# Performance work log

Hardware: AMD Instinct MI355X
Metric: run time of the kernel (lower is better)

The kernel has to match this reference:

```python
import jax, jax.numpy as jnp
import numpy as np
from jax import lax

PART = 224   # PART_IMAGE_SIZE
PAD = 224    # PAD_SIZE
TOPN = 4
IOU_THRESH = 0.25
N_ANCHORS = 1614


def _conv(x, w, b, stride, pad):
    y = lax.conv_general_dilated(x, w, (stride, stride), [(pad, pad), (pad, pad)],
                                 dimension_numbers=('NCHW', 'OIHW', 'NCHW'))
    return y + b[None, :, None, None]


def _iou(box, boxes):
    # box [4], boxes [N,4] as (y0,x0,y1,x1)
    yy0 = jnp.maximum(box[0], boxes[:, 0]); xx0 = jnp.maximum(box[1], boxes[:, 1])
    yy1 = jnp.minimum(box[2], boxes[:, 2]); xx1 = jnp.minimum(box[3], boxes[:, 3])
    inter = jnp.clip(yy1 - yy0, 0.0) * jnp.clip(xx1 - xx0, 0.0)
    a = (box[2] - box[0]) * (box[3] - box[1])
    areas = (boxes[:, 2] - boxes[:, 0]) * (boxes[:, 3] - boxes[:, 1])
    return inter / (a + areas - inter)


def _nms(scores, boxes):
    # hard NMS keeping TOPN boxes; returns indices [TOPN]
    valid = jnp.ones(scores.shape, dtype=bool)
    idxs = []
    for _ in range(TOPN):
        i = jnp.argmax(jnp.where(valid, scores, -jnp.inf))
        idxs.append(i)
        valid = valid & (_iou(boxes[i], boxes) <= IOU_THRESH)
    return jnp.stack(idxs)


def _crop_resize(img, box):
    # img [3,Hp,Wp] padded image, box [4] float; bilinear, align_corners=True,
    # matching F.interpolate(x_pad[:, :, y0:y1, x0:x1], (PART, PART))
    Hp, Wp = img.shape[1], img.shape[2]
    def coords(c0, c1, L):
        t = jnp.arange(PART, dtype=img.dtype) / (PART - 1)
        c = c0 + (c1 - 1.0 - c0) * t          # absolute source coordinate
        cf = jnp.floor(c)
        lo = jnp.clip(cf.astype(jnp.int32), 0, L - 1)
        hi = jnp.clip(lo + 1, 0, L - 1)
        return lo, hi, c - cf
    yl, yh, wy = coords(box[0], box[2], Hp)
    xl, xh, wx = coords(box[1], box[3], Wp)
    g = lambda yi, xi: img[:, yi[:, None], xi[None, :]]   # [3,PART,PART]
    return ((1 - wy)[:, None] * ((1 - wx) * g(yl, xl) + wx * g(yl, xh))
            + wy[:, None] * ((1 - wx) * g(yh, xl) + wx * g(yh, xh)))


def setup_inputs() -> dict:
    key = jax.random.key(0)
    ks = jax.random.split(key, 20)
    x = jax.random.uniform(ks[0], (16, 3, 448, 448), dtype=jnp.float32)
    rpn_feature = jax.random.normal(ks[1], (16, 2048, 14, 14), dtype=jnp.float32)
    # valid boxes inside the padded 896x896 image
    y0 = jax.random.randint(ks[2], (N_ANCHORS,), 0, 560)
    x0 = jax.random.randint(ks[3], (N_ANCHORS,), 0, 560)
    h = jax.random.randint(ks[4], (N_ANCHORS,), 32, 336)
    w = jax.random.randint(ks[5], (N_ANCHORS,), 32, 336)
    anchors = jnp.stack([y0, x0, jnp.minimum(y0 + h, 896), jnp.minimum(x0 + w, 896)], axis=1).astype(jnp.int32)
    s = 0.02
    inp = {
        'x': x, 'rpn_feature': rpn_feature, 'anchors': anchors,
        'w_down1': jax.random.normal(ks[6], (128, 2048, 3, 3), jnp.float32) * s,
        'b_down1': jnp.zeros((128,), jnp.float32),
        'w_down2': jax.random.normal(ks[7], (128, 128, 3, 3), jnp.float32) * s,
        'b_down2': jnp.zeros((128,), jnp.float32),
        'w_down3': jax.random.normal(ks[8], (128, 128, 3, 3), jnp.float32) * s,
        'b_down3': jnp.zeros((128,), jnp.float32),
        'w_tidy1': jax.random.normal(ks[9], (6, 128, 1, 1), jnp.float32) * s,
        'b_tidy1': jnp.zeros((6,), jnp.float32),
        'w_tidy2': jax.random.normal(ks[10], (6, 128, 1, 1), jnp.float32) * s,
        'b_tidy2': jnp.zeros((6,), jnp.float32),
        'w_tidy3': jax.random.normal(ks[11], (9, 128, 1, 1), jnp.float32) * s,
        'b_tidy3': jnp.zeros((9,), jnp.float32),
    }
    return inp


def reference(x, rpn_feature, anchors,
              w_down1, b_down1, w_down2, b_down2, w_down3, b_down3,
              w_tidy1, b_tidy1, w_tidy2, b_tidy2, w_tidy3, b_tidy3):
    B = x.shape[0]
    # ProposalNet
    d1 = jax.nn.relu(_conv(rpn_feature, w_down1, b_down1, 1, 1))   # [B,128,14,14]
    d2 = jax.nn.relu(_conv(d1, w_down2, b_down2, 2, 1))            # [B,128,7,7]
    d3 = jax.nn.relu(_conv(d2, w_down3, b_down3, 2, 1))            # [B,128,4,4]
    t1 = _conv(d1, w_tidy1, b_tidy1, 1, 0).reshape(B, -1)
    t2 = _conv(d2, w_tidy2, b_tidy2, 1, 0).reshape(B, -1)
    t3 = _conv(d3, w_tidy3, b_tidy3, 1, 0).reshape(B, -1)
    rpn_score = jnp.concatenate([t1, t2, t3], axis=1)              # [B, 1614]
    boxes = anchors.astype(x.dtype)                                # [N,4]
    top_n_index = jax.vmap(lambda s: _nms(s, boxes))(rpn_score)    # [B,TOPN]
    top_n_prob = jnp.take_along_axis(rpn_score, top_n_index, axis=1)
    x_pad = jnp.pad(x, ((0, 0), (0, 0), (PAD, PAD), (PAD, PAD)))   # [B,3,896,896]
    sel_boxes = boxes[top_n_index]                                 # [B,TOPN,4]
    part_imgs = jax.vmap(lambda img, bxs: jax.vmap(lambda b: _crop_resize(img, b))(bxs))(x_pad, sel_boxes)
    # part_imgs: [B,TOPN,3,PART,PART]
    return rpn_score, top_n_index, top_n_prob, part_imgs
```

## Files before the change

### kernel.cpp

```cpp
#include <hip/hip_runtime.h>
#include <hip/hip_bf16.h>

#define NB 16
#define NA 1614
#define NBP (NB * 196 * 128)
#define NBP2 (NB * 128 * 49)

typedef __bf16 bf16x8 __attribute__((ext_vector_type(8)));
typedef float f32x4 __attribute__((ext_vector_type(4)));

__device__ __forceinline__ unsigned short f2bf(float v) {
  unsigned u = __float_as_uint(v);
  unsigned r = (u + 0x7FFFu + ((u >> 16) & 1u)) >> 16;
  return (unsigned short)r;
}
__device__ __forceinline__ float bf2f(unsigned short s) {
  return __uint_as_float(((unsigned)s) << 16);
}

__global__ __launch_bounds__(256)
void prep(const float* __restrict__ w, const float* __restrict__ in,
          unsigned short* __restrict__ wTh, unsigned short* __restrict__ wTl,
          unsigned short* __restrict__ aTh, unsigned short* __restrict__ aTl) {
  __shared__ float sbuf[32 * 289];
  const int bid = blockIdx.x;
  if (bid < 1024) {
    const int chunk = bid & 63, b = bid >> 6;
    const float* src = in + ((size_t)b * 2048 + chunk * 32) * 196;
#pragma unroll
    for (int r = 0; r < 7; r++) {
      int e = threadIdx.x + 256 * r;
      if (e < 1568) {
        int ic = e / 49, f = e - ic * 49;
        float4 v = ((const float4*)(src + (size_t)ic * 196))[f];
        float* d = sbuf + ic * 201 + f * 4;
        d[0] = v.x; d[1] = v.y; d[2] = v.z; d[3] = v.w;
      }
    }
    __syncthreads();
    unsigned short* oh = aTh + (size_t)bid * (196 * 32);
    unsigned short* ol = aTl + (size_t)bid * (196 * 32);
#pragma unroll
    for (int r = 0; r < 4; r++) {
      int e = threadIdx.x + 256 * r;
      if (e < 784) {
        int pos = e >> 2, part = e & 3;
        unsigned short hv[8], lv[8];
#pragma unroll
        for (int j = 0; j < 8; j++) {
          float v = sbuf[(part * 8 + j) * 201 + pos];
          unsigned short h = f2bf(v);
          hv[j] = h;
          lv[j] = f2bf(v - bf2f(h));
        }
        ((uint4*)oh)[e] = *(uint4*)hv;
        ((uint4*)ol)[e] = *(uint4*)lv;
      }
    }
  } else {
    const int bid2 = bid - 1024;
    const int ocg = bid2 & 3, ks = (bid2 >> 2) & 3, kcp = bid2 >> 4;
    const int oc0 = ocg * 32;
    const int ic0 = kcp * 128 + ks * 32;
#pragma unroll
    for (int r = 0; r < 9; r++) {
      int f = threadIdx.x + 256 * r;
      int o = f / 72, rem4 = f - o * 72;
      float4 v = *(const float4*)(w + ((size_t)(oc0 + o) * 2048 + ic0) * 9 + rem4 * 4);
      float* d = sbuf + o * 289 + rem4 * 4;
      d[0] = v.x; d[1] = v.y; d[2] = v.z; d[3] = v.w;
    }
    __syncthreads();
#pragma unroll
    for (int r = 0; r < 36; r++) {
      int e = threadIdx.x + 256 * r;
      int tap = e >> 10, rem = e & 1023;
      int o = rem >> 5, ic = rem & 31;
      float v = sbuf[o * 289 + ic * 9 + tap];
      unsigned short h = f2bf(v);
      size_t g2 = ((size_t)(kcp * 36 + tap * 4 + ks) << 12) + oc0 * 32 + rem;
      wTh[g2] = h;
      wTl[g2] = f2bf(v - bf2f(h));
    }
  }
}

#define APL 1360
#define ABUF (4 * APL)

#define LOADB(H, L, T, K)                                                     \
  {                                                                           \
    const size_t o_ = ((size_t)(kc * 36 + (T) * 4 + (K)) << 12) + bln;        \
    const unsigned short* ph_ = wTh + o_;                                     \
    const unsigned short* pq_ = wTl + o_;                                     \
    H[0] = *(const bf16x8*)(ph_);                                             \
    H[1] = *(const bf16x8*)(ph_ + 512);                                       \
    L[0] = *(const bf16x8*)(pq_);                                             \
    L[1] = *(const bf16x8*)(pq_ + 512);                                       \
  }

#define STEP(IT, BUH, BUL, BNH, BNL)                                          \
  {                                                                           \
    const int it_ = (IT);                                                     \
    const int ks_ = it_ / 9, tap_ = it_ - ks_ * 9;                            \
    {             \
      const int ni_ = (it_ < 35) ? it_ + 1 : 35;                              \
      const int nk_ = ni_ / 9, nt_ = ni_ - nk_ * 9;                           \
      LOADB(BNH, BNL, nt_, nk_);                                              \
    }                                                                         \
    if (ks_ < 3) {        \
      if (tap_ == 3 || tap_ == 4) {                                           \
        int e_ = tid + 256 * (tap_ - 3);                                      \
        if (e_ < ne) {                                                        \
          int u_ = pos04 + e_;                                                \
          int pos_ = u_ >> 2, part_ = u_ & 3;                                 \
          int py_ = pos_ / 14, px_ = pos_ - py_ * 14;                         \
          int d_ = (((ks_ + 1) & 1) ? ABUF : 0) + part_ * APL                 \
                   + (py_ + 1 - rowoff) * 136 + (px_ + 1) * 8;                \
          *(uint4*)(sAh + d_) = sgh;                                          \
          *(uint4*)(sAl + d_) = sgl;                                          \
        }                                                                     \
      }                                                                       \
      if (tap_ == 2 || tap_ == 3) {                                           \
        const uint4* gh_ = (const uint4*)(aTh + ((size_t)(b * 64 + kc * 4 + ks_ + 1) * 196) * 32); \
        const uint4* gl_ = (const uint4*)(aTl + ((size_t)(b * 64 + kc * 4 + ks_ + 1) * 196) * 32); \
        int e_ = tid + 256 * (tap_ - 2);                                      \
        if (e_ < ne) { sgh = gh_[pos04 + e_]; sgl = gl_[pos04 + e_]; }        \
      }                                                                       \
    }                                                                         \
    const int t8_ = (tap_ / 3) * 136 + (tap_ - (tap_ / 3) * 3) * 8;           \
    const unsigned short* pah_ = sAh + (ks_ & 1) * ABUF + qoff + t8_;         \
    const unsigned short* pal_ = sAl + (ks_ & 1) * ABUF + qoff + t8_;         \
    bf16x8 afh[7], afl[7];                                                    \
    _Pragma("unroll") for (int mf = 0; mf < 7; mf++) {                        \
      afh[mf] = *(const bf16x8*)(pah_ + abase[mf]);                           \
      afl[mf] = *(const bf16x8*)(pal_ + abase[mf]);                           \
    }                                                                         \
    _Pragma("unroll") for (int mf = 0; mf < 7; mf++)                          \
      _Pragma("unroll") for (int nf = 0; nf < 2; nf++)                        \
        acc[mf][nf] = __builtin_amdgcn_mfma_f32_16x16x32_bf16(afh[mf], BUH[nf], acc[mf][nf], 0, 0, 0); \
    _Pragma("unroll") for (int mf = 0; mf < 7; mf++)                          \
      _Pragma("unroll") for (int nf = 0; nf < 2; nf++)                        \
        acc[mf][nf] = __builtin_amdgcn_mfma_f32_16x16x32_bf16(afl[mf], BUH[nf], acc[mf][nf], 0, 0, 0); \
    _Pragma("unroll") for (int mf = 0; mf < 7; mf++)                          \
      _Pragma("unroll") for (int nf = 0; nf < 2; nf++)                        \
        acc[mf][nf] = __builtin_amdgcn_mfma_f32_16x16x32_bf16(afh[mf], BUL[nf], acc[mf][nf], 0, 0, 0); \
    if (tap_ == 8) __syncthreads();                                           \
  }

__global__ __launch_bounds__(256, 2)
void conv1_mfma(const unsigned short* __restrict__ aTh, const unsigned short* __restrict__ aTl,
                const unsigned short* __restrict__ wTh, const unsigned short* __restrict__ wTl,
                float* __restrict__ p1) {
  const int bid = blockIdx.x;
  const int kc = bid & 15;
  const int b  = (bid >> 4) & 15;
  const int mh = bid >> 8;
  const int tid = threadIdx.x;
  const int wid = tid >> 6, lane = tid & 63;
  const int wn = wid;
  const int q = lane >> 4, ln = lane & 15;

  __shared__ unsigned short sAh[2 * ABUF];
  __shared__ unsigned short sAl[2 * ABUF];

  const int rowoff = 6 * mh;
  const int pos0 = mh ? 98 : 0;
  const int ne   = mh ? 392 : 504;
  const int pos04 = pos0 * 4;

  for (int e = tid; e < 2 * ABUF / 2; e += 256) {
    ((unsigned int*)sAh)[e] = 0u;
    ((unsigned int*)sAl)[e] = 0u;
  }

  int abase[7];
#pragma unroll
  for (int mf = 0; mf < 7; mf++) {
    int row = mh * 112 + mf * 16 + ln;
    int y = row / 14, x = row - y * 14;
    abase[mf] = (row < 196) ? ((y - rowoff) * 136 + x * 8) : 0;
  }
  const int qoff = q * APL;
  const int bln = (wn * 32 + ln) * 32 + q * 8;

  f32x4 acc[7][2];
#pragma unroll
  for (int mf = 0; mf < 7; mf++)
#pragma unroll
    for (int nf = 0; nf < 2; nf++) acc[mf][nf] = (f32x4){0.f, 0.f, 0.f, 0.f};

  uint4 sgh = {}, sgl = {};

  __syncthreads();

  {
    const uint4* gh = (const uint4*)(aTh + ((size_t)(b * 64 + kc * 4) * 196) * 32);
    const uint4* gl = (const uint4*)(aTl + ((size_t)(b * 64 + kc * 4) * 196) * 32);
#pragma unroll
    for (int r = 0; r < 2; r++) {
      int e = tid + 256 * r;
      if (e < ne) {
        int u = pos04 + e;
        int pos = u >> 2, part = u & 3;
        int py = pos / 14, px = pos - py * 14;
        int d = part * APL + (py + 1 - rowoff) * 136 + (px + 1) * 8;
        *(uint4*)(sAh + d) = gh[u];
        *(uint4*)(sAl + d) = gl[u];
      }
    }
  }
  bf16x8 b0h[2], b0l[2], b1h[2], b1l[2];
  LOADB(b0h, b0l, 0, 0);
  __syncthreads();

  for (int it = 0; it < 36; it += 2) {
    STEP(it,     b0h, b0l, b1h, b1l);
    STEP(it + 1, b1h, b1l, b0h, b0l);
  }

  float* pk = p1 + ((size_t)kc * NB + b) * 196 * 128;
#pragma unroll
  for (int mf = 0; mf < 7; mf++) {
    const int row0 = mh * 112 + mf * 16 + q * 4;
#pragma unroll
    for (int nf = 0; nf < 2; nf++) {
      const int oc = wn * 32 + nf * 16 + ln;
#pragma unroll
      for (int r = 0; r < 4; r++) {
        const int row = row0 + r;
        if (row < 196) pk[(size_t)row * 128 + oc] = acc[mf][nf][r];
      }
    }
  }
}

__global__ __launch_bounds__(256)
void conv1_finish_p(const float* __restrict__ p1, const float* __restrict__ bias,
                    float* __restrict__ d1) {
  __shared__ float s[7 * 132];
  const int bid = blockIdx.x;
  const int pt = bid % 28, b = bid / 28;
  const int tid = threadIdx.x;
  if (tid < 224) {
    int pos = tid >> 5, oc4 = tid & 31;
    const float* base = p1 + ((size_t)(b * 196 + pt * 7 + pos)) * 128 + oc4 * 4;
    float4 sum = ((const float4*)bias)[oc4];
#pragma unroll
    for (int k = 0; k < 16; k++) {
      float4 v = *(const float4*)(base + (size_t)k * NBP);
      sum.x += v.x; sum.y += v.y; sum.z += v.z; sum.w += v.w;
    }
    sum.x = fmaxf(sum.x, 0.f); sum.y = fmaxf(sum.y, 0.f);
    sum.z = fmaxf(sum.z, 0.f); sum.w = fmaxf(sum.w, 0.f);
    *(float4*)(s + pos * 132 + oc4 * 4) = sum;
  }
  __syncthreads();
#pragma unroll
  for (int r = 0; r < 4; r++) {
    int e = tid + 256 * r;
    if (e < 896) {
      int oc = e / 7, f = e - oc * 7;
      d1[((size_t)b * 128 + oc) * 196 + pt * 7 + f] = s[f * 132 + oc];
    }
  }
}

__global__ void conv2_part(const float* __restrict__ d1, const float* __restrict__ w,
                           float* __restrict__ p2) {
  const int bid = blockIdx.x;
  const int kc = bid & 3, oct = (bid >> 2) & 3, b = bid >> 4;
  const int ic0 = kc * 32, oc0 = oct * 32;
  const int tid = threadIdx.x;
  const int ocl = tid >> 3, rw = tid & 7;

  __shared__ float s_in[32 * 320];
  __shared__ float s_w[32 * 324];

#pragma unroll
  for (int r = 0; r < 32; r++) {
    const int e = tid + 256 * r;
    const int ch = e >> 8, idx = e & 255;
    const int tr = idx >> 4, tc = idx & 15;
    const int iy = tr - 1, ix = tc - 1;
    float v = 0.f;
    if ((unsigned)iy < 14u && (unsigned)ix < 14u)
      v = d1[((size_t)b * 128 + ic0 + ch) * 196 + iy * 14 + ix];
    s_in[ch * 320 + tr * 20 + tc] = v;
  }
#pragma unroll
  for (int r = 0; r < 36; r++) {
    const int e = tid + 256 * r;
    const int oc = e / 288, rem = e - oc * 288;
    const int ch = rem / 9, tap = rem - ch * 9;
    s_w[ch * 324 + tap * 36 + oc] =
        w[(size_t)(oc0 + oc) * 1152 + (size_t)ic0 * 9 + rem];
  }
  __syncthreads();

  if (rw < 7) {
    float acc[7] = {};
    for (int ic = 0; ic < 32; ic++) {
      const float* wrow = s_w + ic * 324 + ocl;
      const float* irow = s_in + ic * 320;
#pragma unroll
      for (int ky = 0; ky < 3; ky++) {
        const float* r = irow + (2 * rw + ky) * 20;
        const float4 f0 = *(const float4*)(r);
        const float4 f1 = *(const float4*)(r + 4);
        const float4 f2 = *(const float4*)(r + 8);
        const float4 f3 = *(const float4*)(r + 12);
        const float ev[8] = {f0.x, f0.z, f1.x, f1.z, f2.x, f2.z, f3.x, f3.z};
        const float od[7] = {f0.y, f0.w, f1.y, f1.w, f2.y, f2.w, f3.y};
        const float w0 = wrow[(ky * 3 + 0) * 36];
        const float w1 = wrow[(ky * 3 + 1) * 36];
        const float w2 = wrow[(ky * 3 + 2) * 36];
#pragma unroll
        for (int x = 0; x < 7; x++)
          acc[x] = fmaf(w0, ev[x], fmaf(w1, od[x], fmaf(w2, ev[x + 1], acc[x])));
      }
    }
    float* po = p2 + (((size_t)kc * NB + b) * 128 + oc0 + ocl) * 49 + rw * 7;
#pragma unroll
    for (int x = 0; x < 7; x++) po[x] = acc[x];
  }
}

__global__ void conv3_part(const float* __restrict__ p2, const float* __restrict__ bd2,
                           const float* __restrict__ w, float* __restrict__ p3) {
  const int bid = blockIdx.x;
  const int kc = bid & 1, oct = (bid >> 1) & 7, b = bid >> 4;
  const int ic0 = kc * 64, oc0 = oct * 16;
  const int tid = threadIdx.x;
  const int oc = tid >> 4, p = tid & 15;
  const int y = p >> 2, x = p & 3;

  __shared__ float s_in[64 * 108];
  __shared__ float s_w[64 * 144];

#pragma unroll
  for (int r = 0; r < 21; r++) {
    const int e = tid + 256 * r;
    if (e < 64 * 81) {
      const int ch = e / 81, idx = e - ch * 81;
      const int tr = idx / 9, tc = idx - tr * 9;
      const int iy = tr - 1, ix = tc - 1;
      float v = 0.f;
      if ((unsigned)iy < 7u && (unsigned)ix < 7u) {
        const size_t ii = ((size_t)b * 128 + ic0 + ch) * 49 + iy * 7 + ix;
        v = bd2[ic0 + ch] + p2[ii];
        v += p2[(size_t)NBP2 + ii];
        v += p2[(size_t)2 * NBP2 + ii];
        v += p2[(size_t)3 * NBP2 + ii];
        v = fmaxf(v, 0.f);
      }
      s_in[ch * 108 + tr * 12 + tc] = v;
    }
  }
#pragma unroll
  for (int r = 0; r < 36; r++) {
    const int e = tid + 256 * r;
    const int o = e / 576, rem = e - o * 576;
    const int ch = rem / 9, tap = rem - ch * 9;
    s_w[ch * 144 + tap * 16 + o] =
        w[(size_t)(oc0 + o) * 1152 + (size_t)ic0 * 9 + rem];
  }
  __syncthreads();

  float acc = 0.f;
  for (int ic = 0; ic < 64; ic++) {
    const float* wrow = s_w + ic * 144 + oc;
    const float* irow = s_in + ic * 108 + 2 * y * 12 + 2 * x;
#pragma unroll
    for (int ky = 0; ky < 3; ky++)
#pragma unroll
      for (int kx = 0; kx < 3; kx++)
        acc = fmaf(wrow[(ky * 3 + kx) * 16], irow[ky * 12 + kx], acc);
  }
  p3[(((size_t)kc * NB + b) * 128 + oc0 + oc) * 16 + p] = acc;
}

__global__ __launch_bounds__(256, 1)
void score_nms(const float* __restrict__ d1,
               const float* __restrict__ p2, const float* __restrict__ bd2,
               const float* __restrict__ p3, const float* __restrict__ bd3,
               const float* __restrict__ w1, const float* __restrict__ b1,
               const float* __restrict__ w2, const float* __restrict__ b2,
               const float* __restrict__ w3, const float* __restrict__ b3,
               const int* __restrict__ anchors, float* __restrict__ score,
               float* __restrict__ out_idx, float* __restrict__ out_prob,
               float* __restrict__ sel) {
  __shared__ float s_in[32 * 200];
  __shared__ float s_w[21 * 128];
  __shared__ float s_b[21];
  __shared__ float s_sc[NA];
  __shared__ float s_bx[NA * 4];
  __shared__ float r_s[256];
  __shared__ int r_i[256];
  const int b = blockIdx.x, tid = threadIdx.x;

  for (int i = tid; i < 768; i += 256) s_w[i] = w1[i];
  for (int i = tid; i < 768; i += 256) s_w[768 + i] = w2[i];
  for (int i = tid; i < 1152; i += 256) s_w[1536 + i] = w3[i];
  if (tid < 21) s_b[tid] = (tid < 6) ? b1[tid] : (tid < 12) ? b2[tid - 6] : b3[tid - 12];
  for (int i = tid; i < NA; i += 256) {
    s_bx[i * 4 + 0] = (float)anchors[i * 4 + 0];
    s_bx[i * 4 + 1] = (float)anchors[i * 4 + 1];
    s_bx[i * 4 + 2] = (float)anchors[i * 4 + 2];
    s_bx[i * 4 + 3] = (float)anchors[i * 4 + 3];
  }

  float acc[5] = {0.f, 0.f, 0.f, 0.f, 0.f};
  for (int chunk = 0; chunk < 4; chunk++) {
    __syncthreads();
    const float* src = d1 + ((size_t)b * 128 + chunk * 32) * 196;
#pragma unroll
    for (int r = 0; r < 7; r++) {
      int e = tid + 256 * r;
      if (e < 1568) {
        int ic = e / 49, f = e - ic * 49;
        *(float4*)(s_in + ic * 200 + f * 4) = ((const float4*)(src + (size_t)ic * 196))[f];
      }
    }
    __syncthreads();
#pragma unroll
    for (int k = 0; k < 5; k++) {
      int j = tid + 256 * k;
      if (j < 1176) {
        int oc = j / 196, p = j - oc * 196;
        const float* wr = s_w + oc * 128 + chunk * 32;
        float s = acc[k];
#pragma unroll
        for (int ic = 0; ic < 32; ic++) s = fmaf(wr[ic], s_in[ic * 200 + p], s);
        acc[k] = s;
      }
    }
  }
#pragma unroll
  for (int k = 0; k < 5; k++) {
    int j = tid + 256 * k;
    if (j < 1176) {
      int oc = j / 196;
      float s = acc[k] + s_b[oc];
      s_sc[j] = s;
      score[b * NA + j] = s;
    }
  }

  __syncthreads();
  {
    const size_t base = (size_t)b * 6272;
#pragma unroll
    for (int r = 0; r < 7; r++) {
      int e = tid + 256 * r;
      if (e < 1568) {
        const float4 v0 = *(const float4*)(p2 + base + e * 4);
        const float4 v1 = *(const float4*)(p2 + (size_t)NBP2 + base + e * 4);
        const float4 v2 = *(const float4*)(p2 + (size_t)2 * NBP2 + base + e * 4);
        const float4 v3 = *(const float4*)(p2 + (size_t)3 * NBP2 + base + e * 4);
        const float s0[4] = {v0.x, v0.y, v0.z, v0.w};
        const float s1[4] = {v1.x, v1.y, v1.z, v1.w};
        const float s2[4] = {v2.x, v2.y, v2.z, v2.w};
        const float s3[4] = {v3.x, v3.y, v3.z, v3.w};
        float o[4];
#pragma unroll
        for (int k = 0; k < 4; k++) {
          const int oc = (e * 4 + k) / 49;
          float s = bd2[oc] + s0[k];
          s += s1[k]; s += s2[k]; s += s3[k];
          o[k] = fmaxf(s, 0.f);
        }
        float4 vv; vv.x = o[0]; vv.y = o[1]; vv.z = o[2]; vv.w = o[3];
        *(float4*)(s_in + e * 4) = vv;
      }
    }
  }
  __syncthreads();
#pragma unroll
  for (int k = 0; k < 2; k++) {
    int jj = tid + 256 * k;
    if (jj < 294) {
      int oc = jj / 49, p = jj - oc * 49;
      const float* wr = s_w + 768 + oc * 128;
      float s = s_b[6 + oc];
#pragma unroll 8
      for (int ic = 0; ic < 128; ic++) s = fmaf(wr[ic], s_in[ic * 49 + p], s);
      s_sc[1176 + jj] = s;
      score[b * NA + 1176 + jj] = s;
    }
  }

  __syncthreads();
  {
    const float4* s0 = (const float4*)(p3 + (size_t)b * 2048);
    const float4* s1 = (const float4*)(p3 + 32768 + (size_t)b * 2048);
#pragma unroll
    for (int r = 0; r < 2; r++) {
      int e = tid + 256 * r;
      if (e < 512) {
        float4 a = s0[e], c = s1[e];
        float bb = bd3[e >> 2];
        float4 v;
        v.x = fmaxf(a.x + c.x + bb, 0.f);
        v.y = fmaxf(a.y + c.y + bb, 0.f);
        v.z = fmaxf(a.z + c.z + bb, 0.f);
        v.w = fmaxf(a.w + c.w + bb, 0.f);
        *(float4*)(s_in + e * 4) = v;
      }
    }
  }
  __syncthreads();
  if (tid < 144) {
    int oc = tid >> 4, p = tid & 15;
    const float* wr = s_w + 1536 + oc * 128;
    float s = s_b[12 + oc];
#pragma unroll 8
    for (int ic = 0; ic < 128; ic++) s = fmaf(wr[ic], s_in[ic * 16 + p], s);
    s_sc[1470 + tid] = s;
    score[b * NA + 1470 + tid] = s;
  }
  __syncthreads();

  for (int t = 0; t < 4; t++) {
    float bs = -__builtin_inff();
    int bi = NA;
    for (int i = tid; i < NA; i += 256) {
      float s = s_sc[i];
      if (s > bs || (s == bs && i < bi)) { bs = s; bi = i; }
    }
    r_s[tid] = bs; r_i[tid] = bi;
    __syncthreads();
    for (int off = 128; off > 0; off >>= 1) {
      if (tid < off) {
        float s2 = r_s[tid + off]; int i2 = r_i[tid + off];
        if (s2 > r_s[tid] || (s2 == r_s[tid] && i2 < r_i[tid])) { r_s[tid] = s2; r_i[tid] = i2; }
      }
      __syncthreads();
    }
    const int idx = r_i[0];
    const float by0 = s_bx[idx * 4 + 0], bx0 = s_bx[idx * 4 + 1];
    const float by1 = s_bx[idx * 4 + 2], bx1 = s_bx[idx * 4 + 3];
    if (tid == 0) {
      out_idx[b * 4 + t] = (float)idx;
      out_prob[b * 4 + t] = s_sc[idx];
      sel[(b * 4 + t) * 4 + 0] = by0;
      sel[(b * 4 + t) * 4 + 1] = bx0;
      sel[(b * 4 + t) * 4 + 2] = by1;
      sel[(b * 4 + t) * 4 + 3] = bx1;
    }
    __syncthreads();
    const float a = (by1 - by0) * (bx1 - bx0);
    for (int i = tid; i < NA; i += 256) {
      float cy0 = s_bx[i * 4 + 0], cx0 = s_bx[i * 4 + 1];
      float cy1 = s_bx[i * 4 + 2], cx1 = s_bx[i * 4 + 3];
      float yy0 = fmaxf(by0, cy0), xx0 = fmaxf(bx0, cx0);
      float yy1 = fminf(by1, cy1), xx1 = fminf(bx1, cx1);
      float inter = fmaxf(yy1 - yy0, 0.f) * fmaxf(xx1 - xx0, 0.f);
      float ar = (cy1 - cy0) * (cx1 - cx0);
      float iou = inter / (a + ar - inter);
      if (iou > 0.25f) s_sc[i] = -__builtin_inff();
    }
    __syncthreads();
  }
}

__global__ void crop_kernel(const float* __restrict__ x, const float* __restrict__ sel,
                            float* __restrict__ out) {
  int i4 = blockIdx.x * 256 + threadIdx.x;
  const int total4 = NB * 4 * 3 * 224 * 56;
  if (i4 >= total4) return;
  int px0 = (i4 % 56) * 4;
  int t = i4 / 56;
  int py = t % 224; t /= 224;
  int ch = t % 3;  t /= 3;
  int n  = t % 4;
  int b  = t / 4;

  const float* bx = sel + (b * 4 + n) * 4;
  const float y0 = bx[0], x0 = bx[1], y1 = bx[2], x1 = bx[3];

  float ty = (float)py / 223.0f;
  float cy = y0 + (y1 - 1.0f - y0) * ty;
  float cyf = floorf(cy);
  int ylo = (int)cyf; ylo = ylo < 0 ? 0 : (ylo > 895 ? 895 : ylo);
  int yhi = ylo + 1 > 895 ? 895 : ylo + 1;
  float wy = cy - cyf;

  const float* img = x + ((size_t)b * 3 + ch) * 448 * 448;
  auto g = [&](int yy, int xx) -> float {
    yy -= 224; xx -= 224;
    if ((unsigned)yy < 448u && (unsigned)xx < 448u)
      return img[(size_t)yy * 448 + xx];
    return 0.f;
  };

  float4 res;
  float* rp = &res.x;
#pragma unroll
  for (int k = 0; k < 4; k++) {
    float tx = (float)(px0 + k) / 223.0f;
    float cx = x0 + (x1 - 1.0f - x0) * tx;
    float cxf = floorf(cx);
    int xlo = (int)cxf; xlo = xlo < 0 ? 0 : (xlo > 895 ? 895 : xlo);
    int xhi = xlo + 1 > 895 ? 895 : xlo + 1;
    float wx = cx - cxf;
    float v00 = g(ylo, xlo), v01 = g(ylo, xhi);
    float v10 = g(yhi, xlo), v11 = g(yhi, xhi);
    rp[k] = (1.f - wy) * ((1.f - wx) * v00 + wx * v01) +
            wy * ((1.f - wx) * v10 + wx * v11);
  }
  *(float4*)(out + (size_t)i4 * 4) = res;
}

extern "C" void kernel_launch(void* const* d_in, const int* in_sizes, int n_in,
                              void* d_out, int out_size, void* d_ws, size_t ws_size,
                              hipStream_t stream) {
  const float* x    = (const float*)d_in[0];
  const float* rpn  = (const float*)d_in[1];
  const int*   anc  = (const int*)d_in[2];
  const float* w_d1 = (const float*)d_in[3];
  const float* b_d1 = (const float*)d_in[4];
  const float* w_d2 = (const float*)d_in[5];
  const float* b_d2 = (const float*)d_in[6];
  const float* w_d3 = (const float*)d_in[7];
  const float* b_d3 = (const float*)d_in[8];
  const float* w_t1 = (const float*)d_in[9];
  const float* b_t1 = (const float*)d_in[10];
  const float* w_t2 = (const float*)d_in[11];
  const float* b_t2 = (const float*)d_in[12];
  const float* w_t3 = (const float*)d_in[13];
  const float* b_t3 = (const float*)d_in[14];

  float* out = (float*)d_out;
  float* ws = (float*)d_ws;

  float* d1  = ws;
  float* d2  = d1 + 401408;
  float* d3  = d2 + 100352;
  float* sel = d3 + 32768;
  float* p2  = sel + 256;
  float* p3  = p2 + 401408;
  unsigned short* wTh = (unsigned short*)(p3 + 65536);
  unsigned short* wTl = wTh + 2359296;
  unsigned short* aTh = wTl + 2359296;
  unsigned short* aTl = aTh + 6422528;

  float* score    = out;
  float* out_idx  = out + 25824;
  float* out_prob = out + 25888;
  float* parts    = out + 25952;
  float* p1       = parts;

  prep<<<dim3(1280), dim3(256), 0, stream>>>(w_d1, rpn, wTh, wTl, aTh, aTl);
  conv1_mfma<<<dim3(512), dim3(256), 0, stream>>>(aTh, aTl, wTh, wTl, p1);
  conv1_finish_p<<<dim3(448), dim3(256), 0, stream>>>(p1, b_d1, d1);
  conv2_part<<<dim3(256), dim3(256), 0, stream>>>(d1, w_d2, p2);
  conv3_part<<<dim3(256), dim3(256), 0, stream>>>(p2, b_d2, w_d3, p3);
  score_nms<<<dim3(16), dim3(256), 0, stream>>>(d1, p2, b_d2, p3, b_d3, w_t1, b_t1, w_t2, b_t2,
                                                w_t3, b_t3, anc, score, out_idx, out_prob, sel);
  crop_kernel<<<dim3(9408), dim3(256), 0, stream>>>(x, sel, parts);
}
```

Baseline: 279.2 us.

## Retile conv1 MFMA kernel into quarter-row blocks with 2 waves of 64 channels

The conv1 implicit-GEMM kernel is re-tiled. Each block now covers a quarter of the 196 spatial positions (49 rows padded to 64) with 128 threads, and each wave computes 64 output channels instead of 32. The launch grid doubles to 1024 blocks. The aim is better occupancy and load balance, plus more B-fragment reuse per A load. In exchange, more rows are wasted to padding (49 of 64 used), the halo loads per block overlap more, and the weight-fragment registers double.

Measured after the change: 285.6 us. +2.3%, slower.

```diff
diff --git a/kernel.cpp b/kernel.cpp
--- a/kernel.cpp
+++ b/kernel.cpp
@@ -85,7 +85,7 @@
   }
 }
 
-#define APL 1360
+#define APL 816
 #define ABUF (4 * APL)
 
 #define LOADB(H, L, T, K)                                                     \
@@ -95,8 +95,12 @@
     const unsigned short* pq_ = wTl + o_;                                     \
     H[0] = *(const bf16x8*)(ph_);                                             \
     H[1] = *(const bf16x8*)(ph_ + 512);                                       \
+    H[2] = *(const bf16x8*)(ph_ + 1024);                                      \
+    H[3] = *(const bf16x8*)(ph_ + 1536);                                      \
     L[0] = *(const bf16x8*)(pq_);                                             \
     L[1] = *(const bf16x8*)(pq_ + 512);                                       \
+    L[2] = *(const bf16x8*)(pq_ + 1024);                                      \
+    L[3] = *(const bf16x8*)(pq_ + 1536);                                      \
   }
 
 #define STEP(IT, BUH, BUL, BNH, BNL)                                          \
@@ -108,87 +112,92 @@
       const int nk_ = ni_ / 9, nt_ = ni_ - nk_ * 9;                           \
       LOADB(BNH, BNL, nt_, nk_);                                              \
     }                                                                         \
-    if (ks_ < 3) {        \
-      if (tap_ == 3 || tap_ == 4) {                                           \
-        int e_ = tid + 256 * (tap_ - 3);                                      \
-        if (e_ < ne) {                                                        \
-          int u_ = pos04 + e_;                                                \
+    if (ks_ < 3) {  \
+      if (tap_ >= 3 && tap_ <= 5) {                                           \
+        int e_ = tid + 128 * (tap_ - 3);                                      \
+        if (e_ < ecount) {                                                    \
+          int u_ = e0 + e_;                                                   \
           int pos_ = u_ >> 2, part_ = u_ & 3;                                 \
           int py_ = pos_ / 14, px_ = pos_ - py_ * 14;                         \
           int d_ = (((ks_ + 1) & 1) ? ABUF : 0) + part_ * APL                 \
-                   + (py_ + 1 - rowoff) * 136 + (px_ + 1) * 8;                \
+                   + (py_ - row0) * 136 + (px_ + 1) * 8;                      \
           *(uint4*)(sAh + d_) = sgh;                                          \
           *(uint4*)(sAl + d_) = sgl;                                          \
         }                                                                     \
       }                                                                       \
-      if (tap_ == 2 || tap_ == 3) {                                           \
+      if (tap_ >= 2 && tap_ <= 4) {                                           \
         const uint4* gh_ = (const uint4*)(aTh + ((size_t)(b * 64 + kc * 4 + ks_ + 1) * 196) * 32); \
         const uint4* gl_ = (const uint4*)(aTl + ((size_t)(b * 64 + kc * 4 + ks_ + 1) * 196) * 32); \
-        int e_ = tid + 256 * (tap_ - 2);                                      \
-        if (e_ < ne) { sgh = gh_[pos04 + e_]; sgl = gl_[pos04 + e_]; }        \
+        int e_ = tid + 128 * (tap_ - 2);                                      \
+        if (e_ < ecount) { sgh = gh_[e0 + e_]; sgl = gl_[e0 + e_]; }          \
       }                                                                       \
     }                                                                         \
     const int t8_ = (tap_ / 3) * 136 + (tap_ - (tap_ / 3) * 3) * 8;           \
     const unsigned short* pah_ = sAh + (ks_ & 1) * ABUF + qoff + t8_;         \
     const unsigned short* pal_ = sAl + (ks_ & 1) * ABUF + qoff + t8_;         \
-    bf16x8 afh[7], afl[7];                                                    \
-    _Pragma("unroll") for (int mf = 0; mf < 7; mf++) {                        \
+    bf16x8 afh[4], afl[4];                                                    \
+    _Pragma("unroll") for (int mf = 0; mf < 4; mf++) {                        \
       afh[mf] = *(const bf16x8*)(pah_ + abase[mf]);                           \
       afl[mf] = *(const bf16x8*)(pal_ + abase[mf]);                           \
     }                                                                         \
-    _Pragma("unroll") for (int mf = 0; mf < 7; mf++)                          \
-      _Pragma("unroll") for (int nf = 0; nf < 2; nf++)                        \
+    _Pragma("unroll") for (int mf = 0; mf < 4; mf++)                          \
+      _Pragma("unroll") for (int nf = 0; nf < 4; nf++)                        \
         acc[mf][nf] = __builtin_amdgcn_mfma_f32_16x16x32_bf16(afh[mf], BUH[nf], acc[mf][nf], 0, 0, 0); \
-    _Pragma("unroll") for (int mf = 0; mf < 7; mf++)                          \
-      _Pragma("unroll") for (int nf = 0; nf < 2; nf++)                        \
+    _Pragma("unroll") for (int mf = 0; mf < 4; mf++)                          \
+      _Pragma("unroll") for (int nf = 0; nf < 4; nf++)                        \
         acc[mf][nf] = __builtin_amdgcn_mfma_f32_16x16x32_bf16(afl[mf], BUH[nf], acc[mf][nf], 0, 0, 0); \
-    _Pragma("unroll") for (int mf = 0; mf < 7; mf++)                          \
-      _Pragma("unroll") for (int nf = 0; nf < 2; nf++)                        \
+    _Pragma("unroll") for (int mf = 0; mf < 4; mf++)                          \
+      _Pragma("unroll") for (int nf = 0; nf < 4; nf++)                        \
         acc[mf][nf] = __builtin_amdgcn_mfma_f32_16x16x32_bf16(afh[mf], BUL[nf], acc[mf][nf], 0, 0, 0); \
     if (tap_ == 8) __syncthreads();                                           \
   }
 
-__global__ __launch_bounds__(256, 2)
+__global__ __launch_bounds__(128, 2)
 void conv1_mfma(const unsigned short* __restrict__ aTh, const unsigned short* __restrict__ aTl,
                 const unsigned short* __restrict__ wTh, const unsigned short* __restrict__ wTl,
                 float* __restrict__ p1) {
   const int bid = blockIdx.x;
   const int kc = bid & 15;
   const int b  = (bid >> 4) & 15;
-  const int mh = bid >> 8;
+  const int mq = bid >> 8;
   const int tid = threadIdx.x;
-  const int wid = tid >> 6, lane = tid & 63;
-  const int wn = wid;
+  const int wn = tid >> 6, lane = tid & 63;
   const int q = lane >> 4, ln = lane & 15;
 
   __shared__ unsigned short sAh[2 * ABUF];
   __shared__ unsigned short sAl[2 * ABUF];
 
-  const int rowoff = 6 * mh;
-  const int pos0 = mh ? 98 : 0;
-  const int ne   = mh ? 392 : 504;
-  const int pos04 = pos0 * 4;
-
-  for (int e = tid; e < 2 * ABUF / 2; e += 256) {
+  const int row0 = (mq == 0) ? -1 : (mq == 1) ? 2 : (mq == 2) ? 6 : 9;
+  const int y0 = (row0 < 0) ? 0 : row0;
+  const int y1 = (row0 + 5 > 13) ? 13 : row0 + 5;
+  const int e0 = y0 * 56;
+  const int ecount = (y1 - y0 + 1) * 56;
+
+  for (int e = tid; e < ABUF; e += 128) {
     ((unsigned int*)sAh)[e] = 0u;
     ((unsigned int*)sAl)[e] = 0u;
   }
 
-  int abase[7];
-#pragma unroll
-  for (int mf = 0; mf < 7; mf++) {
-    int row = mh * 112 + mf * 16 + ln;
-    int y = row / 14, x = row - y * 14;
-    abase[mf] = (row < 196) ? ((y - rowoff) * 136 + x * 8) : 0;
+  int abase[4];
+#pragma unroll
+  for (int mf = 0; mf < 4; mf++) {
+    int lrow = mf * 16 + ln;
+    if (lrow < 49) {
+      int grow = mq * 49 + lrow;
+      int y = grow / 14, x = grow - y * 14;
+      abase[mf] = (y - 1 - row0) * 136 + x * 8;
+    } else {
+      abase[mf] = 0;
+    }
   }
   const int qoff = q * APL;
-  const int bln = (wn * 32 + ln) * 32 + q * 8;
-
-  f32x4 acc[7][2];
-#pragma unroll
-  for (int mf = 0; mf < 7; mf++)
-#pragma unroll
-    for (int nf = 0; nf < 2; nf++) acc[mf][nf] = (f32x4){0.f, 0.f, 0.f, 0.f};
+  const int bln = (wn * 64 + ln) * 32 + q * 8;
+
+  f32x4 acc[4][4];
+#pragma unroll
+  for (int mf = 0; mf < 4; mf++)
+#pragma unroll
+    for (int nf = 0; nf < 4; nf++) acc[mf][nf] = (f32x4){0.f, 0.f, 0.f, 0.f};
 
   uint4 sgh = {}, sgl = {};
 
@@ -198,19 +207,19 @@
     const uint4* gh = (const uint4*)(aTh + ((size_t)(b * 64 + kc * 4) * 196) * 32);
     const uint4* gl = (const uint4*)(aTl + ((size_t)(b * 64 + kc * 4) * 196) * 32);
 #pragma unroll
-    for (int r = 0; r < 2; r++) {
-      int e = tid + 256 * r;
-      if (e < ne) {
-        int u = pos04 + e;
+    for (int r = 0; r < 3; r++) {
+      int e = tid + 128 * r;
+      if (e < ecount) {
+        int u = e0 + e;
         int pos = u >> 2, part = u & 3;
         int py = pos / 14, px = pos - py * 14;
-        int d = part * APL + (py + 1 - rowoff) * 136 + (px + 1) * 8;
+        int d = part * APL + (py - row0) * 136 + (px + 1) * 8;
         *(uint4*)(sAh + d) = gh[u];
         *(uint4*)(sAl + d) = gl[u];
       }
     }
   }
-  bf16x8 b0h[2], b0l[2], b1h[2], b1l[2];
+  bf16x8 b0h[4], b0l[4], b1h[4], b1l[4];
   LOADB(b0h, b0l, 0, 0);
   __syncthreads();
 
@@ -221,15 +230,14 @@
 
   float* pk = p1 + ((size_t)kc * NB + b) * 196 * 128;
 #pragma unroll
-  for (int mf = 0; mf < 7; mf++) {
-    const int row0 = mh * 112 + mf * 16 + q * 4;
-#pragma unroll
-    for (int nf = 0; nf < 2; nf++) {
-      const int oc = wn * 32 + nf * 16 + ln;
+  for (int mf = 0; mf < 4; mf++) {
+#pragma unroll
+    for (int nf = 0; nf < 4; nf++) {
+      const int oc = wn * 64 + nf * 16 + ln;
 #pragma unroll
       for (int r = 0; r < 4; r++) {
-        const int row = row0 + r;
-        if (row < 196) pk[(size_t)row * 128 + oc] = acc[mf][nf][r];
+        const int lrow = mf * 16 + q * 4 + r;
+        if (lrow < 49) pk[(size_t)(mq * 49 + lrow) * 128 + oc] = acc[mf][nf][r];
       }
     }
   }
@@ -652,7 +660,7 @@
   float* p1       = parts;
 
   prep<<<dim3(1280), dim3(256), 0, stream>>>(w_d1, rpn, wTh, wTl, aTh, aTl);
-  conv1_mfma<<<dim3(512), dim3(256), 0, stream>>>(aTh, aTl, wTh, wTl, p1);
+  conv1_mfma<<<dim3(1024), dim3(128), 0, stream>>>(aTh, aTl, wTh, wTl, p1);
   conv1_finish_p<<<dim3(448), dim3(256), 0, stream>>>(p1, b_d1, d1);
   conv2_part<<<dim3(256), dim3(256), 0, stream>>>(d1, w_d2, p2);
   conv3_part<<<dim3(256), dim3(256), 0, stream>>>(p2, b_d2, w_d3, p3);
```
